# Optimization experiments

Measured on AMD Instinct MI355X. Metric: run time of the kernel, lower is better.

The kernel has to match this reference:

```python
import jax, jax.numpy as jnp
import numpy as np

N_NODES = 30000
N_EDGES = 300000
N_GRAPHS = 512
SEQ = 1000
HEADS = 10
CH = 78


def setup_inputs() -> dict:
    key = jax.random.key(0)
    ks = jax.random.split(key, 20)
    def w(k, shape, scale=0.02):
        return jax.random.normal(k, shape, jnp.float32) * scale
    x = jax.random.normal(ks[0], (N_NODES, CH), jnp.float32)
    edge_index = jax.random.randint(ks[1], (2, N_EDGES), 0, N_NODES, jnp.int32)
    # every graph gets a contiguous block of nodes (sorted batch vector)
    batch = (jnp.arange(N_NODES) * N_GRAPHS // N_NODES).astype(jnp.int32)
    target = jax.random.randint(ks[2], (N_GRAPHS, SEQ), 0, 26, jnp.int32)
    return {
        "x": x, "edge_index": edge_index, "batch": batch, "target": target,
        "W_gat": w(ks[3], (CH, HEADS * CH)),
        "att_src": w(ks[4], (HEADS, CH), 0.1),
        "att_dst": w(ks[5], (HEADS, CH), 0.1),
        "b_gat": jnp.zeros((HEADS * CH,), jnp.float32),
        "W_gcn": w(ks[6], (HEADS * CH, HEADS * CH)),
        "b_gcn": jnp.zeros((HEADS * CH,), jnp.float32),
        "W_fcg1": w(ks[7], (2 * HEADS * CH, 1500)), "b_fcg1": jnp.zeros((1500,), jnp.float32),
        "W_fcg2": w(ks[8], (1500, 128)), "b_fcg2": jnp.zeros((128,), jnp.float32),
        "emb": w(ks[9], (26, 128), 1.0),
        "W_conv": w(ks[10], (32, 1000, 8)), "b_conv": jnp.zeros((32,), jnp.float32),
        "W_fcxt": w(ks[11], (32 * 121, 128)), "b_fcxt": jnp.zeros((128,), jnp.float32),
        "W_fc1": w(ks[12], (256, 1024)), "b_fc1": jnp.zeros((1024,), jnp.float32),
        "W_fc2": w(ks[13], (1024, 512)), "b_fc2": jnp.zeros((512,), jnp.float32),
        "W_out": w(ks[14], (512, 1)), "b_out": jnp.zeros((1,), jnp.float32),
    }


def reference(x, edge_index, batch, target,
              W_gat, att_src, att_dst, b_gat, W_gcn, b_gcn,
              W_fcg1, b_fcg1, W_fcg2, b_fcg2, emb, W_conv, b_conv,
              W_fcxt, b_fcxt, W_fc1, b_fc1, W_fc2, b_fc2, W_out, b_out):
    N = x.shape[0]
    loop = jnp.arange(N, dtype=edge_index.dtype)
    src = jnp.concatenate([edge_index[0], loop])  # self-loops (PyG default)
    dst = jnp.concatenate([edge_index[1], loop])

    # ---- GATConv(78 -> 78, heads=10, concat) ----
    h = (x @ W_gat).reshape(N, HEADS, CH)           # [N,H,C]
    a_s = jnp.einsum('nhc,hc->nh', h, att_src)      # [N,H]
    a_d = jnp.einsum('nhc,hc->nh', h, att_dst)
    logits = jax.nn.leaky_relu(a_s[src] + a_d[dst], 0.2)   # [E',H]
    m = jax.ops.segment_max(logits, dst, num_segments=N)
    e = jnp.exp(logits - m[dst])
    denom = jax.ops.segment_sum(e, dst, num_segments=N)
    alpha = e / (denom[dst] + 1e-16)                # per-dst softmax
    xg = jax.ops.segment_sum(h[src] * alpha[:, :, None], dst, num_segments=N)
    xg = jax.nn.relu(xg.reshape(N, HEADS * CH) + b_gat)

    # ---- GCNConv(780 -> 780), symmetric norm with self-loops ----
    deg = jax.ops.segment_sum(jnp.ones_like(dst, dtype=xg.dtype), dst, num_segments=N)
    dinv = jax.lax.rsqrt(jnp.maximum(deg, 1.0))
    norm = dinv[src] * dinv[dst]                    # [E']
    xw = xg @ W_gcn
    xg = jax.ops.segment_sum(xw[src] * norm[:, None], dst, num_segments=N) + b_gcn
    xg = jax.nn.relu(xg)

    # ---- global max + mean pooling per graph ----
    gmax = jax.ops.segment_max(xg, batch, num_segments=N_GRAPHS)
    cnt = jax.ops.segment_sum(jnp.ones((N,), xg.dtype), batch, num_segments=N_GRAPHS)
    gmean = jax.ops.segment_sum(xg, batch, num_segments=N_GRAPHS) / cnt[:, None]
    xp = jnp.concatenate([gmax, gmean], axis=1)     # [G,1560]
    xp = jax.nn.relu(xp @ W_fcg1 + b_fcg1)          # dropout = identity (eval)
    xp = xp @ W_fcg2 + b_fcg2                       # [G,128]

    # ---- protein branch ----
    xt = emb[target]                                # [G,1000,128]
    conv = jax.lax.conv_general_dilated(
        xt, W_conv, window_strides=(1,), padding='VALID',
        dimension_numbers=('NCH', 'OIH', 'NCH'))    # [G,32,121]
    conv = conv + b_conv[None, :, None]
    xt = conv.reshape(conv.shape[0], -1) @ W_fcxt + b_fcxt  # [G,128]

    # ---- joint MLP ----
    xc = jnp.concatenate([xp, xt], axis=1)          # [G,256]
    xc = jax.nn.relu(xc @ W_fc1 + b_fc1)
    xc = jax.nn.relu(xc @ W_fc2 + b_fc2)
    return xc @ W_out + b_out                       # [G,1]
```

## Files before the change

kernel.cpp:

```cpp
#include <hip/hip_runtime.h>
#include <hip/hip_bf16.h>
#include <cstdint>
#include <cstddef>

#define N_NODES 30000
#define E0      300000
#define EPRIME  330000
#define NG      512
#define SEQL    1000
#define HEADS   10
#define CHN     78
#define HC      780
#define HP      800
#define MAXD    64

typedef __attribute__((ext_vector_type(8))) short bf16x8;
typedef __attribute__((ext_vector_type(4))) float f32x4;
typedef __attribute__((ext_vector_type(8))) unsigned short u16x8;

static __device__ __forceinline__ int src_of(const int* ei, int e){
  return (e < E0) ? ei[e] : (e - E0);
}
static __device__ __forceinline__ int dst_of(const int* ei, int e){
  return (e < E0) ? ei[E0 + e] : (e - E0);
}
static __device__ __forceinline__ unsigned short f2bf(float f){
  union { float f; unsigned u; } a; a.f = f;
  unsigned r = a.u + 0x7fff + ((a.u >> 16) & 1);
  return (unsigned short)(r >> 16);
}
static __device__ __forceinline__ float bf2f(unsigned short u){
  union { unsigned u; float f; } a; a.u = ((unsigned)u) << 16; return a.f;
}
static __device__ __forceinline__ void gl_lds16(const unsigned short* g, unsigned short* l){
  __builtin_amdgcn_global_load_lds(
      (const __attribute__((address_space(1))) void*)g,
      (__attribute__((address_space(3))) void*)l,
      16, 0, 0);
}

__global__ void k_bucket(const int* __restrict__ ei, int* __restrict__ cnt, int* __restrict__ bkt){
  int e = blockIdx.x*256 + threadIdx.x;
  if (e < EPRIME){
    int d = dst_of(ei, e);
    int s = src_of(ei, e);
    int slot = atomicAdd(&cnt[d], 1);
    if (slot < MAXD) bkt[d*MAXD + slot] = s;
  }
}

__global__ __launch_bounds__(256) void k_w2t(const float* __restrict__ W_conv, float* __restrict__ w2t){
  int b = blockIdx.x;
  int o = threadIdx.x >> 3, k = threadIdx.x & 7;
  w2t[(size_t)b*256 + threadIdx.x] = W_conv[(size_t)o*8000 + b*8 + k];
}

static __device__ void transp_tile(const float* __restrict__ src, unsigned short* __restrict__ dst,
                                   int K, int N, int Kp, int bx, int by, int hpad){
  __shared__ float t[32][33];
  int k0 = bx*32, n0 = by*32;
  int c = threadIdx.x & 31, r = threadIdx.x >> 5;
  #pragma unroll
  for (int i=0;i<4;i++){
    int k = k0 + r + i*8;
    float v = 0.f;
    if (k < K && n0 + c < N) v = src[(size_t)k*N + n0 + c];
    t[r + i*8][c] = v;
  }
  __syncthreads();
  #pragma unroll
  for (int i=0;i<4;i++){
    int nn = n0 + r + i*8;
    int kk = k0 + c;
    if (nn < N){
      if (hpad){
        if (kk < K){
          int hh = kk/78;
          dst[(size_t)nn*Kp + hh*80 + (kk - hh*78)] = f2bf(t[c][r + i*8]);
        }
      } else {
        if (kk < Kp) dst[(size_t)nn*Kp + kk] = f2bf(t[c][r + i*8]);
      }
    }
  }
}

static __device__ void conv_body(int g, int tid, const int* __restrict__ target,
                                 const float* __restrict__ W2t, const float* __restrict__ emb,
                                 const float* __restrict__ b_conv, float* __restrict__ convf){
  int pg = tid & 7;
  __shared__ int   tgt[SEQL];
  __shared__ int   cntv[26];
  __shared__ int   startv[27];
  __shared__ int   ofs[26];
  __shared__ alignas(16) unsigned short posv[SEQL];
  __shared__ float sE[26*128 + 32];

  for (int i = tid; i < 26*128; i += 256) sE[i] = emb[i];
  if (tid < 32) sE[26*128 + tid] = 0.f;
  if (tid < 26) cntv[tid] = 0;
  const int* tg = target + g*SEQL;
  for (int i = tid; i < SEQL; i += 256) tgt[i] = tg[i];
  __syncthreads();
  for (int i = tid; i < SEQL; i += 256) atomicAdd(&cntv[tgt[i]], 1);
  __syncthreads();
  if (tid == 0){
    int s = 0;
    #pragma unroll
    for (int v = 0; v < 26; v++){ startv[v] = s; ofs[v] = s; s += cntv[v]; }
    startv[26] = s;
  }
  __syncthreads();
  for (int i = tid; i < SEQL; i += 256){
    int v = tgt[i];
    int slot = atomicAdd(&ofs[v], 1);
    posv[slot] = (unsigned short)i;
  }
  __syncthreads();

  const float* wp2 = W2t + tid;
  int p0 = pg * 16;
  int np = 121 - p0; if (np > 16) np = 16;
  int lb = (tid & 63) & 56;
  float acc[16];
  #pragma unroll
  for (int i=0;i<16;i++) acc[i]=0.f;

  for (int v = 0; v < 26; v++){
    int jb = startv[v], je = startv[v+1];
    float s = 0.f;
    for (int j = jb; j < je; j += 8){
      float w[8];
      #pragma unroll
      for (int q = 0; q < 8; q++){
        int idx = j + q;
        int p = (int)posv[(idx < je) ? idx : jb];
        float val = wp2[p << 8];
        w[q] = (idx < je) ? val : 0.f;
      }
      #pragma unroll
      for (int q = 0; q < 8; q++) s += w[q];
    }
    float u[8];
    #pragma unroll
    for (int k = 0; k < 8; k++) u[k] = __shfl(s, lb + k, 64);
    const float* ep = &sE[v*128 + p0];
    float e[24];
    #pragma unroll
    for (int i2=0;i2<24;i2+=4){
      float4 q4 = *(const float4*)(ep + i2);
      e[i2]=q4.x; e[i2+1]=q4.y; e[i2+2]=q4.z; e[i2+3]=q4.w;
    }
    #pragma unroll
    for (int pl=0; pl<16; pl++){
      acc[pl] += u[0]*e[pl]   + u[1]*e[pl+1] + u[2]*e[pl+2] + u[3]*e[pl+3]
               + u[4]*e[pl+4] + u[5]*e[pl+5] + u[6]*e[pl+6] + u[7]*e[pl+7];
    }
  }
  int o = tid >> 3;
  float bo = b_conv[o];
  for (int pl=0; pl<np; pl++)
    convf[(size_t)g*3872 + o*121 + p0 + pl] = acc[pl] + bo;
}

__global__ __launch_bounds__(256) void k_prep(
    const float* __restrict__ x, unsigned short* __restrict__ xb,
    const float* __restrict__ W_gat, unsigned short* __restrict__ wgat_t,
    const float* __restrict__ W_gcn, unsigned short* __restrict__ wgcn_t,
    const float* __restrict__ W_fcg1, unsigned short* __restrict__ wfcg1_t,
    const int* __restrict__ target, const float* __restrict__ w2t,
    const float* __restrict__ emb, const float* __restrict__ b_conv, float* __restrict__ convf,
    unsigned short* __restrict__ xwbp,
    float* __restrict__ xc, float* __restrict__ t1, float* __restrict__ t2, float* __restrict__ fg1,
    const float* __restrict__ b_fcg2, const float* __restrict__ b_fcxt,
    const float* __restrict__ b_fc1, const float* __restrict__ b_fc2,
    const float* __restrict__ b_fcg1, int* __restrict__ cnt)
{
  int b = blockIdx.x;
  int tid = threadIdx.x;
  if (b < 512){ conv_body(b, tid, target, w2t, emb, b_conv, convf); return; }
  b -= 512;
  if (b < 11250){
    int idx = b*256 + tid;
    if (idx < N_NODES*96){
      int n = idx/96, k = idx - n*96;
      xb[idx] = (k < CHN) ? f2bf(x[(size_t)n*CHN + k]) : 0;
    }
    return;
  }
  b -= 11250;
  if (b < 75){ transp_tile(W_gat, wgat_t, CHN, HC, 96, b%3, b/3, 0); return; }
  b -= 75;
  if (b < 625){ transp_tile(W_gcn, wgcn_t, HC, HC, HP, b%25, b/25, 1); return; }
  b -= 625;
  if (b < 2303){ transp_tile(W_fcg1, wfcg1_t, 1560, 1500, 1568, b%49, b/49, 0); return; }
  b -= 2303;
  {
    int g = b;
    int zi = g*256 + tid;
    if (zi < N_NODES) cnt[zi] = 0;
    if (tid < 128){
      xc[(size_t)g*256 + tid]       = b_fcg2[tid];
      xc[(size_t)g*256 + 128 + tid] = b_fcxt[tid];
    }
    for (int i = tid; i < 1024; i += 256) t1[(size_t)g*1024 + i] = b_fc1[i];
    for (int i = tid; i < 512;  i += 256) t2[(size_t)g*512  + i] = b_fc2[i];
    for (int i = tid; i < 1500; i += 256) fg1[(size_t)g*1500 + i] = b_fcg1[i];
    for (int i = tid; i < 59; i += 256){
      int n = g + i*512;
      if (n < N_NODES)
        *reinterpret_cast<unsigned long long*>(xwbp + (size_t)n*HP + HC) = 0ull;
    }
    if (zi < 7800){
      int nn = zi/10, p = zi - (zi/10)*10;
      *reinterpret_cast<unsigned*>(wgcn_t + (size_t)nn*HP + p*80 + 78) = 0u;
    }
  }
}

__global__ __launch_bounds__(256) void k_mfma_bt(
    const unsigned short* __restrict__ A, const unsigned short* __restrict__ Bt,
    const float* __restrict__ bias, float* __restrict__ C, unsigned short* __restrict__ Cb,
    int M, int N, int Kp, int ldc, int relu,
    int ntc, int ntr, int ntk, int Kc, int accum, int hpad)
{
  const int total = ntc*ntr*ntk;
  const int per = (total + 7) >> 3;
  const int b = blockIdx.x;
  const int w = (b & 7)*per + (b >> 3);
  if (w >= total) return;
  const int kt = w / (ntc*ntr);
  const int r2 = w - kt*(ntc*ntr);
  const int row_t = r2 / ntc, col_t = r2 - row_t*ntc;
  const int row0 = row_t*128, col0 = col_t*128;
  const int kbeg = kt*Kc;
  const int kend = min(kbeg + Kc, Kp);

  __shared__ unsigned short As[2][128*32];
  __shared__ unsigned short Bs[2][128*32];
  const int tid = threadIdx.x;
  const int lane = tid & 63;
  const int wv = tid >> 6;
  const int wm = wv >> 1, wn = wv & 1;
  const int quad = lane >> 4, l16 = lane & 15;
  const int srow = lane >> 2;
  const int cidx = lane & 3;
  const int scol = (cidx ^ (srow & 3)) * 8;

  f32x4 acc[4][4];
  #pragma unroll
  for (int mi=0;mi<4;mi++)
    #pragma unroll
    for (int ni=0;ni<4;ni++){
      acc[mi][ni][0]=0.f; acc[mi][ni][1]=0.f; acc[mi][ni][2]=0.f; acc[mi][ni][3]=0.f;
    }

  auto stage = [&](int bsel, int kk){
    #pragma unroll
    for (int i=0;i<2;i++){
      int ch = wv*2 + i;
      int r  = ch*16 + srow;
      gl_lds16(A  + (size_t)(row0 + r)*Kp + kk + scol, &As[bsel][ch*512]);
      gl_lds16(Bt + (size_t)(col0 + r)*Kp + kk + scol, &Bs[bsel][ch*512]);
    }
  };

  const int nt = (kend - kbeg) >> 5;
  stage(0, kbeg);
  __syncthreads();
  int cur = 0;
  for (int t = 0; t < nt; ++t){
    if (t+1 < nt) stage(cur^1, kbeg + ((t+1) << 5));
    bf16x8 af[4], bfr[4];
    #pragma unroll
    for (int mi=0;mi<4;mi++)
      af[mi]  = *(const bf16x8*)(&As[cur][(wm*64 + mi*16 + l16)*32 + ((quad ^ (l16 & 3))*8)]);
    #pragma unroll
    for (int ni=0;ni<4;ni++)
      bfr[ni] = *(const bf16x8*)(&Bs[cur][(wn*64 + ni*16 + l16)*32 + ((quad ^ (l16 & 3))*8)]);
    #pragma unroll
    for (int mi=0;mi<4;mi++)
      #pragma unroll
      for (int ni=0;ni<4;ni++)
        acc[mi][ni] = __builtin_amdgcn_mfma_f32_16x16x32_bf16(af[mi], bfr[ni], acc[mi][ni], 0,0,0);
    __syncthreads();
    cur ^= 1;
  }

  #pragma unroll
  for (int mi=0;mi<4;mi++){
    #pragma unroll
    for (int rr=0;rr<4;rr++){
      int row = row0 + wm*64 + mi*16 + quad*4 + rr;
      if (row >= M) continue;
      #pragma unroll
      for (int ni=0;ni<4;ni++){
        int col = col0 + wn*64 + ni*16 + l16;
        if (col >= N) continue;
        float v = acc[mi][ni][rr];
        if (accum){
          atomicAdd(&C[(size_t)row*ldc + col], v);
        } else {
          if (bias) v += bias[col];
          if (relu) v = fmaxf(v, 0.f);
          int cs = col;
          if (hpad){ int hh = col/78; cs = hh*80 + (col - hh*78); }
          if (Cb) Cb[(size_t)row*ldc + cs] = f2bf(v);
          else    C [(size_t)row*ldc + cs] = v;
        }
      }
    }
  }
}

__global__ __launch_bounds__(256) void k_gemm_sk(const float* __restrict__ A, const float* __restrict__ B,
    float* __restrict__ C, int M, int N, int K, int lda, int ldb, int ldc, int Kc, int relu_a)
{
  __shared__ float As[16][34];
  __shared__ float Bs[16][64];
  const int tid = threadIdx.x;
  const int tx = tid & 15, ty = tid >> 4;
  const int row0 = blockIdx.y * 32, col0 = blockIdx.x * 64;
  const int kbeg = blockIdx.z * Kc;
  const int kend = min(kbeg + Kc, K);
  float acc[2][4];
  #pragma unroll
  for (int i=0;i<2;i++)
    #pragma unroll
    for (int j=0;j<4;j++) acc[i][j] = 0.f;

  for (int k0 = kbeg; k0 < kend; k0 += 16){
    #pragma unroll
    for (int i=0;i<2;i++){
      int idx = tid + i*256;
      int r = idx >> 4, c = idx & 15;
      int gr = row0 + r, gc = k0 + c;
      float v = (gr < M && gc < kend) ? A[(size_t)gr*lda + gc] : 0.f;
      if (relu_a) v = fmaxf(v, 0.f);
      As[c][r] = v;
    }
    #pragma unroll
    for (int i=0;i<4;i++){
      int idx = tid + i*256;
      int r = idx >> 6, c = idx & 63;
      int gr = k0 + r, gc = col0 + c;
      Bs[r][c] = (gr < kend && gc < N) ? B[(size_t)gr*ldb + gc] : 0.f;
    }
    __syncthreads();
    #pragma unroll
    for (int kk=0; kk<16; kk++){
      float a0 = As[kk][ty*2], a1 = As[kk][ty*2+1];
      float b0 = Bs[kk][tx*4], b1 = Bs[kk][tx*4+1], b2 = Bs[kk][tx*4+2], b3 = Bs[kk][tx*4+3];
      acc[0][0]+=a0*b0; acc[0][1]+=a0*b1; acc[0][2]+=a0*b2; acc[0][3]+=a0*b3;
      acc[1][0]+=a1*b0; acc[1][1]+=a1*b1; acc[1][2]+=a1*b2; acc[1][3]+=a1*b3;
    }
    __syncthreads();
  }
  #pragma unroll
  for (int i=0;i<2;i++){
    int r = row0 + ty*2 + i;
    if (r >= M) continue;
    #pragma unroll
    for (int j=0;j<4;j++){
      int c = col0 + tx*4 + j;
      if (c < N) atomicAdd(&C[(size_t)r*ldc + c], acc[i][j]);
    }
  }
}

__global__ __launch_bounds__(256) void k_attn(const unsigned short* __restrict__ hb,
    const float* __restrict__ att_src, const float* __restrict__ att_dst,
    float* __restrict__ a_s, float* __restrict__ a_d){
  __shared__ float ssrc[HC], sdst[HC];
  for (int i = threadIdx.x; i < HC; i += 256){ ssrc[i]=att_src[i]; sdst[i]=att_dst[i]; }
  __syncthreads();
  int idx = blockIdx.x*256 + threadIdx.x;
  if (idx >= N_NODES*HEADS) return;
  int n  = idx / HEADS;
  int hh = idx - n*HEADS;
  const unsigned* hp2 = (const unsigned*)(hb + (size_t)n*HP + hh*80);
  const float* as_ = ssrc + hh*CHN;
  const float* ad_ = sdst + hh*CHN;
  float s1=0.f, s2=0.f;
  #pragma unroll 13
  for (int c2=0;c2<39;c2++){
    unsigned u = hp2[c2];
    float v0 = bf2f((unsigned short)(u & 0xffffu));
    float v1 = bf2f((unsigned short)(u >> 16));
    int c = 2*c2;
    s1 += v0*as_[c] + v1*as_[c+1];
    s2 += v0*ad_[c] + v1*ad_[c+1];
  }
  a_s[idx]=s1; a_d[idx]=s2;
}

__global__ __launch_bounds__(256) void k_gat_agg(
    const unsigned short* __restrict__ hb, const float* __restrict__ a_s, const float* __restrict__ a_d,
    const float* __restrict__ b_gat, const int* __restrict__ cnt, const int* __restrict__ bkt,
    unsigned short* __restrict__ xgb, float* __restrict__ dinv)
{
  int half = threadIdx.x >> 7;
  int lt   = threadIdx.x & 127;
  int n = blockIdx.x*2 + half;
  int deg = cnt[n];
  int degc = min(deg, MAXD);
  __shared__ int   s_src[2][MAXD];
  __shared__ float s_adn[2][HEADS];
  __shared__ float s_lg[2][MAXD*HEADS];
  __shared__ float s_al[2][MAXD*HEADS];
  if (lt < HEADS) s_adn[half][lt] = a_d[(size_t)n*HEADS + lt];
  if (lt < degc)  s_src[half][lt] = bkt[n*MAXD + lt];
  __syncthreads();
  for (int idx = lt; idx < degc*HEADS; idx += 128){
    int j = idx/HEADS, t = idx - j*HEADS;
    float l = a_s[(size_t)s_src[half][j]*HEADS + t] + s_adn[half][t];
    s_lg[half][idx] = (l > 0.f) ? l : 0.2f*l;
  }
  __syncthreads();
  if (lt < HEADS){
    float m = -3.4e38f;
    for (int j=0;j<degc;j++) m = fmaxf(m, s_lg[half][j*HEADS+lt]);
    float s = 0.f;
    for (int j=0;j<degc;j++){ float e = __expf(s_lg[half][j*HEADS+lt]-m); s_al[half][j*HEADS+lt]=e; s+=e; }
    float inv = 1.f/(s + 1e-16f);
    for (int j=0;j<degc;j++) s_al[half][j*HEADS+lt] *= inv;
  }
  __syncthreads();
  if (lt < 100){
    int h = lt/10;
    int r = lt - h*10;
    int nv = (r==9) ? 6 : 8;
    int chb = h*CHN + r*8;
    const float* alp = &s_al[half][h];
    float acc[8];
    #pragma unroll
    for (int e=0;e<8;e++) acc[e]=0.f;
    auto ld = [&](int j, uint4& v, float& a){
      int s = s_src[half][j];
      a = alp[j*HEADS];
      v = *((const uint4*)(hb + (size_t)s*HP) + lt);
    };
    auto fm = [&](const uint4& v, float a){
      unsigned uu[4] = {v.x, v.y, v.z, v.w};
      #pragma unroll
      for (int e2=0;e2<4;e2++){
        acc[2*e2]   += a*bf2f((unsigned short)(uu[e2] & 0xffffu));
        acc[2*e2+1] += a*bf2f((unsigned short)(uu[e2] >> 16));
      }
    };
    int j = 0;
    for (; j+4 <= degc; j += 4){
      uint4 v0,v1,v2,v3; float a0,a1,a2,a3;
      ld(j,v0,a0); ld(j+1,v1,a1); ld(j+2,v2,a2); ld(j+3,v3,a3);
      fm(v0,a0); fm(v1,a1); fm(v2,a2); fm(v3,a3);
    }
    if (j+2 <= degc){
      uint4 v0,v1; float a0,a1;
      ld(j,v0,a0); ld(j+1,v1,a1);
      fm(v0,a0); fm(v1,a1);
      j += 2;
    }
    if (j < degc){
      uint4 v0; float a0;
      ld(j,v0,a0); fm(v0,a0);
    }
    u16x8 o;
    #pragma unroll
    for (int e=0;e<8;e++){
      float ov = (e < nv) ? fmaxf(acc[e] + b_gat[chb+e], 0.f) : 0.f;
      o[e] = f2bf(ov);
    }
    *((u16x8*)(xgb + (size_t)n*HP) + lt) = o;
  }
  if (lt == 0) dinv[n] = rsqrtf((float)deg);
}

__global__ __launch_bounds__(256) void k_gcn_agg(
    const unsigned short* __restrict__ xwb, const float* __restrict__ dinv, const float* __restrict__ b_gcn,
    const int* __restrict__ cnt, const int* __restrict__ bkt,
    unsigned short* __restrict__ xg2b)
{
  int half = threadIdx.x >> 7;
  int lt   = threadIdx.x & 127;
  int n = blockIdx.x*2 + half;
  int deg = min(cnt[n], MAXD);
  __shared__ int   s_src[2][MAXD];
  __shared__ float s_w[2][MAXD];
  if (lt < deg){
    int s = bkt[n*MAXD + lt];
    s_src[half][lt] = s;
    s_w[half][lt] = dinv[s];
  }
  __syncthreads();
  if (lt < 98){
    int ch0 = lt*8;
    float acc[8];
    #pragma unroll
    for (int e=0;e<8;e++) acc[e]=0.f;
    auto ld = [&](int j, uint4& v, float& a){
      int s = s_src[half][j];
      a = s_w[half][j];
      v = *((const uint4*)(xwb + (size_t)s*HP) + lt);
    };
    auto fm = [&](const uint4& v, float a){
      unsigned uu[4] = {v.x, v.y, v.z, v.w};
      #pragma unroll
      for (int e2=0;e2<4;e2++){
        acc[2*e2]   += a*bf2f((unsigned short)(uu[e2] & 0xffffu));
        acc[2*e2+1] += a*bf2f((unsigned short)(uu[e2] >> 16));
      }
    };
    int j = 0;
    for (; j+4 <= deg; j += 4){
      uint4 v0,v1,v2,v3; float a0,a1,a2,a3;
      ld(j,v0,a0); ld(j+1,v1,a1); ld(j+2,v2,a2); ld(j+3,v3,a3);
      fm(v0,a0); fm(v1,a1); fm(v2,a2); fm(v3,a3);
    }
    if (j+2 <= deg){
      uint4 v0,v1; float a0,a1;
      ld(j,v0,a0); ld(j+1,v1,a1);
      fm(v0,a0); fm(v1,a1);
      j += 2;
    }
    if (j < deg){
      uint4 v0; float a0;
      ld(j,v0,a0); fm(v0,a0);
    }
    float dn = dinv[n];
    ushort4 o0, o1;
    float r0 = fmaxf(dn*acc[0] + ((ch0   < HC) ? b_gcn[ch0  ] : 0.f), 0.f);
    float r1 = fmaxf(dn*acc[1] + ((ch0+1 < HC) ? b_gcn[ch0+1] : 0.f), 0.f);
    float r2 = fmaxf(dn*acc[2] + ((ch0+2 < HC) ? b_gcn[ch0+2] : 0.f), 0.f);
    float r3 = fmaxf(dn*acc[3] + ((ch0+3 < HC) ? b_gcn[ch0+3] : 0.f), 0.f);
    float r4 = fmaxf(dn*acc[4] + ((ch0+4 < HC) ? b_gcn[ch0+4] : 0.f), 0.f);
    float r5 = fmaxf(dn*acc[5] + ((ch0+5 < HC) ? b_gcn[ch0+5] : 0.f), 0.f);
    float r6 = fmaxf(dn*acc[6] + ((ch0+6 < HC) ? b_gcn[ch0+6] : 0.f), 0.f);
    float r7 = fmaxf(dn*acc[7] + ((ch0+7 < HC) ? b_gcn[ch0+7] : 0.f), 0.f);
    o0.x=f2bf(r0); o0.y=f2bf(r1); o0.z=f2bf(r2); o0.w=f2bf(r3);
    o1.x=f2bf(r4); o1.y=f2bf(r5); o1.z=f2bf(r6); o1.w=f2bf(r7);
    unsigned short* row = xg2b + (size_t)n*HC;
    *(ushort4*)(row + ch0) = o0;
    if (ch0+4 < HC) *(ushort4*)(row + ch0+4) = o1;
  }
}

__global__ __launch_bounds__(256) void k_pool(const unsigned short* __restrict__ xg2b,
                                              unsigned short* __restrict__ xpb){
  int g = blockIdx.x;
  int n0 = (N_NODES*g + NG-1) >> 9;
  int n1 = (N_NODES*(g+1) + NG-1) >> 9;
  float inv = 1.f/(float)(n1 - n0);
  int c4 = threadIdx.x;
  if (c4 < 195){
    const ushort4* x4 = (const ushort4*)xg2b;
    float m0=-3.4e38f,m1=-3.4e38f,m2=-3.4e38f,m3=-3.4e38f;
    float s0=0.f,s1=0.f,s2=0.f,s3=0.f;
    for (int n = n0; n < n1; n++){
      ushort4 v = x4[(size_t)n*195 + c4];
      float a=bf2f(v.x), b=bf2f(v.y), c=bf2f(v.z), d=bf2f(v.w);
      m0=fmaxf(m0,a); m1=fmaxf(m1,b); m2=fmaxf(m2,c); m3=fmaxf(m3,d);
      s0+=a; s1+=b; s2+=c; s3+=d;
    }
    int ch = 4*c4;
    unsigned short* row = xpb + (size_t)g*1568;
    row[ch]=f2bf(m0); row[ch+1]=f2bf(m1); row[ch+2]=f2bf(m2); row[ch+3]=f2bf(m3);
    row[HC+ch]=f2bf(s0*inv); row[HC+ch+1]=f2bf(s1*inv);
    row[HC+ch+2]=f2bf(s2*inv); row[HC+ch+3]=f2bf(s3*inv);
  }
  if (threadIdx.x < 8) xpb[(size_t)g*1568 + 1560 + threadIdx.x] = 0;
}

__global__ __launch_bounds__(64) void k_final(const float* __restrict__ t2, const float* __restrict__ W_out,
                                              const float* __restrict__ b_out, float* __restrict__ out){
  int g = blockIdx.x;
  int lane = threadIdx.x;
  const float* r = t2 + (size_t)g*512;
  float s = 0.f;
  #pragma unroll
  for (int i = lane; i < 512; i += 64) s += fmaxf(r[i], 0.f)*W_out[i];
  #pragma unroll
  for (int off=32; off; off>>=1) s += __shfl_down(s, off);
  if (lane==0) out[g] = s + b_out[0];
}

extern "C" void kernel_launch(void* const* d_in, const int* in_sizes, int n_in,
                              void* d_out, int out_size, void* d_ws, size_t ws_size,
                              hipStream_t stream) {
  const float* x      = (const float*)d_in[0];
  const int*   ei     = (const int*)  d_in[1];
  const int*   target = (const int*)  d_in[3];
  const float* W_gat  = (const float*)d_in[4];
  const float* att_src= (const float*)d_in[5];
  const float* att_dst= (const float*)d_in[6];
  const float* b_gat  = (const float*)d_in[7];
  const float* W_gcn  = (const float*)d_in[8];
  const float* b_gcn  = (const float*)d_in[9];
  const float* W_fcg1 = (const float*)d_in[10];
  const float* b_fcg1 = (const float*)d_in[11];
  const float* W_fcg2 = (const float*)d_in[12];
  const float* b_fcg2 = (const float*)d_in[13];
  const float* emb    = (const float*)d_in[14];
  const float* W_conv = (const float*)d_in[15];
  const float* b_conv = (const float*)d_in[16];
  const float* W_fcxt = (const float*)d_in[17];
  const float* b_fcxt = (const float*)d_in[18];
  const float* W_fc1  = (const float*)d_in[19];
  const float* b_fc1  = (const float*)d_in[20];
  const float* W_fc2  = (const float*)d_in[21];
  const float* b_fc2  = (const float*)d_in[22];
  const float* W_out  = (const float*)d_in[23];
  const float* b_out  = (const float*)d_in[24];
  float* out = (float*)d_out;

  char* ws = (char*)d_ws;
  size_t off = 0;
  auto alloc = [&](size_t bytes)->char*{
    char* p = ws + off;
    off += (bytes + 255) & ~(size_t)255;
    return p;
  };
  unsigned short* hb  = (unsigned short*)alloc((size_t)N_NODES*HP*2);
  unsigned short* xwb = (unsigned short*)alloc((size_t)N_NODES*HP*2);
  unsigned short* xu  = (unsigned short*)alloc((size_t)N_NODES*HP*2);
  unsigned short* xb     = (unsigned short*)alloc((size_t)N_NODES*96*2);
  unsigned short* wgat_t = (unsigned short*)alloc((size_t)HC*96*2);
  unsigned short* wgcn_t = (unsigned short*)alloc((size_t)HC*HP*2);
  unsigned short* wfcg1_t= (unsigned short*)alloc((size_t)1500*1568*2);
  unsigned short* xpb    = (unsigned short*)alloc((size_t)NG*1568*2);
  float* a_s    = (float*)alloc((size_t)N_NODES*HEADS*4);
  float* a_d    = (float*)alloc((size_t)N_NODES*HEADS*4);
  float* dinv   = (float*)alloc((size_t)N_NODES*4);
  int*   cnt    = (int*)  alloc((size_t)N_NODES*4);
  int*   bkt    = (int*)  alloc((size_t)N_NODES*MAXD*4);
  float* fg1    = (float*)alloc((size_t)NG*1500*4);
  float* convf  = (float*)alloc((size_t)NG*3872*4);
  float* xc     = (float*)alloc((size_t)NG*256*4);
  float* t1     = (float*)alloc((size_t)NG*1024*4);
  float* t2     = (float*)alloc((size_t)NG*512*4);
  float* w2t    = (float*)alloc((size_t)SEQL*256*4);

  unsigned short* xgb  = xu;
  unsigned short* xg2b = xu;

  k_w2t<<<1000, 256, 0, stream>>>(W_conv, w2t);

  k_prep<<<512+11250+75+625+2303+512, 256, 0, stream>>>(
      x, xb, W_gat, wgat_t, W_gcn, wgcn_t, W_fcg1, wfcg1_t,
      target, w2t, emb, b_conv, convf, xwb,
      xc, t1, t2, fg1, b_fcg2, b_fcxt, b_fc1, b_fc2, b_fcg1, cnt);

  k_bucket<<<(EPRIME+255)/256, 256, 0, stream>>>(ei, cnt, bkt);

  auto swgrid = [](int total){ return 8 * ((total + 7) / 8); };

  k_mfma_bt<<<swgrid(7*235), 256, 0, stream>>>(xb, wgat_t, nullptr, nullptr, hb,
                                               N_NODES, HC, 96, HP, 0, 7, 235, 1, 96, 0, 1);
  k_attn<<<(N_NODES*HEADS+255)/256, 256, 0, stream>>>(hb, att_src, att_dst, a_s, a_d);
  k_gat_agg<<<N_NODES/2, 256, 0, stream>>>(hb, a_s, a_d, b_gat, cnt, bkt, xgb, dinv);

  k_mfma_bt<<<swgrid(7*235), 256, 0, stream>>>(xgb, wgcn_t, nullptr, nullptr, xwb,
                                               N_NODES, HC, HP, HP, 0, 7, 235, 1, HP, 0, 0);
  k_gcn_agg<<<N_NODES/2, 256, 0, stream>>>(xwb, dinv, b_gcn, cnt, bkt, xg2b);

  k_pool<<<NG, 256, 0, stream>>>(xg2b, xpb);
  k_mfma_bt<<<swgrid(12*4*2), 256, 0, stream>>>(xpb, wfcg1_t, nullptr, fg1, nullptr,
                                                NG, 1500, 1568, 1500, 0, 12, 4, 2, 800, 1, 0);
  k_gemm_sk<<<dim3(2, 16, 8), 256, 0, stream>>>(fg1, W_fcg2, xc, NG, 128, 1500, 1500, 128, 256, 192, 1);

  k_gemm_sk<<<dim3(2, 16, 8), 256, 0, stream>>>(convf, W_fcxt, xc + 128, NG, 128, 3872, 3872, 128, 256, 512, 0);

  k_gemm_sk<<<dim3(16, 16, 1), 256, 0, stream>>>(xc, W_fc1, t1, NG, 1024, 256, 256, 1024, 1024, 256, 0);
  k_gemm_sk<<<dim3(8, 16, 2), 256, 0, stream>>>(t1, W_fc2, t2, NG, 512, 1024, 1024, 512, 512, 512, 1);
  k_final<<<NG, 64, 0, stream>>>(t2, W_out, b_out, out);
}
```

Baseline: 805.2 us.

## Fold bucketing into prep, merge two split-K GEMMs, raise split-K factors

```diff
diff --git a/kernel.cpp b/kernel.cpp
--- a/kernel.cpp
+++ b/kernel.cpp
@@ -39,20 +39,13 @@
       16, 0, 0);
 }
 
-__global__ void k_bucket(const int* __restrict__ ei, int* __restrict__ cnt, int* __restrict__ bkt){
-  int e = blockIdx.x*256 + threadIdx.x;
-  if (e < EPRIME){
-    int d = dst_of(ei, e);
-    int s = src_of(ei, e);
-    int slot = atomicAdd(&cnt[d], 1);
-    if (slot < MAXD) bkt[d*MAXD + slot] = s;
-  }
-}
-
-__global__ __launch_bounds__(256) void k_w2t(const float* __restrict__ W_conv, float* __restrict__ w2t){
+__global__ __launch_bounds__(256) void k_w2t(const float* __restrict__ W_conv, float* __restrict__ w2t,
+                                             int* __restrict__ cnt){
   int b = blockIdx.x;
   int o = threadIdx.x >> 3, k = threadIdx.x & 7;
   w2t[(size_t)b*256 + threadIdx.x] = W_conv[(size_t)o*8000 + b*8 + k];
+  int zi = b*256 + threadIdx.x;
+  if (zi < N_NODES) cnt[zi] = 0;
 }
 
 static __device__ void transp_tile(const float* __restrict__ src, unsigned short* __restrict__ dst,
@@ -174,7 +167,8 @@
     float* __restrict__ xc, float* __restrict__ t1, float* __restrict__ t2, float* __restrict__ fg1,
     const float* __restrict__ b_fcg2, const float* __restrict__ b_fcxt,
     const float* __restrict__ b_fc1, const float* __restrict__ b_fc2,
-    const float* __restrict__ b_fcg1, int* __restrict__ cnt)
+    const float* __restrict__ b_fcg1,
+    const int* __restrict__ ei, int* __restrict__ cnt, int* __restrict__ bkt)
 {
   int b = blockIdx.x;
   int tid = threadIdx.x;
@@ -195,10 +189,9 @@
   b -= 625;
   if (b < 2303){ transp_tile(W_fcg1, wfcg1_t, 1560, 1500, 1568, b%49, b/49, 0); return; }
   b -= 2303;
-  {
+  if (b < 512){
     int g = b;
     int zi = g*256 + tid;
-    if (zi < N_NODES) cnt[zi] = 0;
     if (tid < 128){
       xc[(size_t)g*256 + tid]       = b_fcg2[tid];
       xc[(size_t)g*256 + 128 + tid] = b_fcxt[tid];
@@ -214,6 +207,17 @@
     if (zi < 7800){
       int nn = zi/10, p = zi - (zi/10)*10;
       *reinterpret_cast<unsigned*>(wgcn_t + (size_t)nn*HP + p*80 + 78) = 0u;
+    }
+    return;
+  }
+  b -= 512;
+  {
+    int e = b*256 + tid;
+    if (e < EPRIME){
+      int d = dst_of(ei, e);
+      int s = src_of(ei, e);
+      int slot = atomicAdd(&cnt[d], 1);
+      if (slot < MAXD) bkt[d*MAXD + slot] = s;
     }
   }
 }
@@ -313,15 +317,16 @@
   }
 }
 
-__global__ __launch_bounds__(256) void k_gemm_sk(const float* __restrict__ A, const float* __restrict__ B,
-    float* __restrict__ C, int M, int N, int K, int lda, int ldb, int ldc, int Kc, int relu_a)
+static __device__ void gemm_sk_body(const float* __restrict__ A, const float* __restrict__ B,
+    float* __restrict__ C, int M, int N, int K, int lda, int ldb, int ldc, int Kc, int relu_a,
+    int bx, int by, int bz)
 {
   __shared__ float As[16][34];
   __shared__ float Bs[16][64];
   const int tid = threadIdx.x;
   const int tx = tid & 15, ty = tid >> 4;
-  const int row0 = blockIdx.y * 32, col0 = blockIdx.x * 64;
-  const int kbeg = blockIdx.z * Kc;
+  const int row0 = by * 32, col0 = bx * 64;
+  const int kbeg = bz * Kc;
   const int kend = min(kbeg + Kc, K);
   float acc[2][4];
   #pragma unroll
@@ -366,6 +371,28 @@
       if (c < N) atomicAdd(&C[(size_t)r*ldc + c], acc[i][j]);
     }
   }
+}
+
+__global__ __launch_bounds__(256) void k_gemm_sk(const float* __restrict__ A, const float* __restrict__ B,
+    float* __restrict__ C, int M, int N, int K, int lda, int ldb, int ldc, int Kc, int relu_a)
+{
+  gemm_sk_body(A, B, C, M, N, K, lda, ldb, ldc, Kc, relu_a,
+               blockIdx.x, blockIdx.y, blockIdx.z);
+}
+
+__global__ __launch_bounds__(256) void k_gemm_dual(
+    const float* __restrict__ A1, const float* __restrict__ B1, float* __restrict__ C1,
+    int K1, int lda1, int ldb1, int ldc1, int Kc1, int relu1, int nz1,
+    const float* __restrict__ A2, const float* __restrict__ B2, float* __restrict__ C2,
+    int K2, int lda2, int ldb2, int ldc2, int Kc2, int relu2)
+{
+  const float *A, *B; float* C; int K, lda, ldb, ldc, Kc, relu, z;
+  if ((int)blockIdx.z < nz1){
+    A=A1; B=B1; C=C1; K=K1; lda=lda1; ldb=ldb1; ldc=ldc1; Kc=Kc1; relu=relu1; z=blockIdx.z;
+  } else {
+    A=A2; B=B2; C=C2; K=K2; lda=lda2; ldb=ldb2; ldc=ldc2; Kc=Kc2; relu=relu2; z=blockIdx.z-nz1;
+  }
+  gemm_sk_body(A, B, C, NG, 128, K, lda, ldb, ldc, Kc, relu, blockIdx.x, blockIdx.y, z);
 }
 
 __global__ __launch_bounds__(256) void k_attn(const unsigned short* __restrict__ hb,
@@ -642,14 +669,13 @@
   unsigned short* xgb  = xu;
   unsigned short* xg2b = xu;
 
-  k_w2t<<<1000, 256, 0, stream>>>(W_conv, w2t);
-
-  k_prep<<<512+11250+75+625+2303+512, 256, 0, stream>>>(
+  k_w2t<<<1000, 256, 0, stream>>>(W_conv, w2t, cnt);
+
+  k_prep<<<512+11250+75+625+2303+512+1290, 256, 0, stream>>>(
       x, xb, W_gat, wgat_t, W_gcn, wgcn_t, W_fcg1, wfcg1_t,
       target, w2t, emb, b_conv, convf, xwb,
-      xc, t1, t2, fg1, b_fcg2, b_fcxt, b_fc1, b_fc2, b_fcg1, cnt);
-
-  k_bucket<<<(EPRIME+255)/256, 256, 0, stream>>>(ei, cnt, bkt);
+      xc, t1, t2, fg1, b_fcg2, b_fcxt, b_fc1, b_fc2, b_fcg1,
+      ei, cnt, bkt);
 
   auto swgrid = [](int total){ return 8 * ((total + 7) / 8); };
 
@@ -663,13 +689,13 @@
   k_gcn_agg<<<N_NODES/2, 256, 0, stream>>>(xwb, dinv, b_gcn, cnt, bkt, xg2b);
 
   k_pool<<<NG, 256, 0, stream>>>(xg2b, xpb);
-  k_mfma_bt<<<swgrid(12*4*2), 256, 0, stream>>>(xpb, wfcg1_t, nullptr, fg1, nullptr,
-                                                NG, 1500, 1568, 1500, 0, 12, 4, 2, 800, 1, 0);
-  k_gemm_sk<<<dim3(2, 16, 8), 256, 0, stream>>>(fg1, W_fcg2, xc, NG, 128, 1500, 1500, 128, 256, 192, 1);
-
-  k_gemm_sk<<<dim3(2, 16, 8), 256, 0, stream>>>(convf, W_fcxt, xc + 128, NG, 128, 3872, 3872, 128, 256, 512, 0);
-
-  k_gemm_sk<<<dim3(16, 16, 1), 256, 0, stream>>>(xc, W_fc1, t1, NG, 1024, 256, 256, 1024, 1024, 256, 0);
-  k_gemm_sk<<<dim3(8, 16, 2), 256, 0, stream>>>(t1, W_fc2, t2, NG, 512, 1024, 1024, 512, 512, 512, 1);
+  k_mfma_bt<<<swgrid(12*4*4), 256, 0, stream>>>(xpb, wfcg1_t, nullptr, fg1, nullptr,
+                                                NG, 1500, 1568, 1500, 0, 12, 4, 4, 416, 1, 0);
+  k_gemm_dual<<<dim3(2, 16, 32), 256, 0, stream>>>(
+      fg1,   W_fcg2, xc,       1500, 1500, 128, 256,  96, 1, 16,
+      convf, W_fcxt, xc + 128, 3872, 3872, 128, 256, 248, 0);
+
+  k_gemm_sk<<<dim3(16, 16, 2), 256, 0, stream>>>(xc, W_fc1, t1, NG, 1024, 256, 256, 1024, 1024, 128, 0);
+  k_gemm_sk<<<dim3(8, 16, 4), 256, 0, stream>>>(t1, W_fc2, t2, NG, 512, 1024, 1024, 512, 512, 256, 1);
   k_final<<<NG, 64, 0, stream>>>(t2, W_out, b_out, out);
 }
```

Result: faster. 704.0 us (-12.6%).
